# Kernel optimization log

Hardware: AMD Instinct MI355X
Metric: run time of the kernel (lower is better)

Reference implementation:

```python
import jax, jax.numpy as jnp
import numpy as np

B, S, D, H = 2, 4096, 512, 8
HD = D // H  # head_dim = 64


def setup_inputs() -> dict:
    key = jax.random.key(0)
    ks = jax.random.split(key, 7)
    scale = 1.0 / np.sqrt(D)
    return {
        "x": jax.random.normal(ks[0], (B, S, D), dtype=jnp.float32),
        "Wq": jax.random.uniform(ks[1], (D, D), jnp.float32, -scale, scale),
        "bq": jax.random.uniform(ks[2], (D,), jnp.float32, -scale, scale),
        "Wk": jax.random.uniform(ks[3], (D, D), jnp.float32, -scale, scale),
        "bk": jax.random.uniform(ks[4], (D,), jnp.float32, -scale, scale),
        "Wv": jax.random.uniform(ks[5], (D, D), jnp.float32, -scale, scale),
        "bv": jax.random.uniform(ks[6], (D,), jnp.float32, -scale, scale),
    }


def reference(x, Wq, bq, Wk, bk, Wv, bv):
    # torch Linear: y = x @ W.T + b
    q = x @ Wq.T + bq  # [B,S,D]
    k = x @ Wk.T + bk
    v = x @ Wv.T + bv
    # split heads -> [B,H,S,HD]
    q = q.reshape(B, S, H, HD).transpose(0, 2, 1, 3)
    k = k.reshape(B, S, H, HD).transpose(0, 2, 1, 3)
    v = v.reshape(B, S, H, HD).transpose(0, 2, 1, 3)
    # NOTE: module scales by sqrt(pitch_dim), NOT sqrt(head_dim) -- keep faithful.
    scores = jnp.einsum("bhqd,bhkd->bhqk", q, k) / jnp.sqrt(jnp.float32(D))
    causal = jnp.tril(jnp.ones((S, S), dtype=bool))  # lower-tri incl. diag allowed
    scores = jnp.where(causal, scores, -jnp.inf)
    attn = jax.nn.softmax(scores, axis=-1)
    out = jnp.einsum("bhqk,bhkd->bhqd", attn, v)  # [B,H,S,HD]
    return out.transpose(0, 2, 1, 3).reshape(B, S, D)
```

## Files before the change

### kernel.cpp

```cpp
#include <hip/hip_runtime.h>
#include <hip/hip_bf16.h>
#include <math.h>

#define BB 2
#define SS 4096
#define DD 512
#define HH 8
#define HD 64
#define MSD (BB*SS*DD)
#define WSZ (DD*DD)

#define XOFF (4*(size_t)MSD)
#define WOFF (5*(size_t)MSD)
#define POFF (3*(size_t)MSD)

typedef __attribute__((ext_vector_type(8))) short bf16x8;
typedef __attribute__((ext_vector_type(4))) float f32x4;

__device__ __forceinline__ unsigned short f2bf(float f) {
    unsigned int u = __float_as_uint(f);
    u += 0x7fff + ((u >> 16) & 1);
    return (unsigned short)(u >> 16);
}
__device__ __forceinline__ unsigned int pk2bf(float a, float b) {
    __hip_bfloat162 h = __float22bfloat162_rn(make_float2(a, b));
    union { __hip_bfloat162 h2; unsigned int u; } cv; cv.h2 = h;
    return cv.u;
}

#define GLD16(gsrc, ldst) \
    __builtin_amdgcn_global_load_lds((const __attribute__((address_space(1))) unsigned int*)(gsrc), \
                                     (__attribute__((address_space(3))) unsigned int*)(ldst), 16, 0, 0)

#define CH(qb,t0,t1) ((unsigned)(qb) | ((unsigned)(t0)<<8) | ((unsigned)(t1)<<16))
__device__ __constant__ unsigned int SCHED[48] = {
  CH(31,0,32),  CH(31,32,64), CH(0,0,2),
  CH(15,0,32),  CH(29,0,30),  CH(1,0,4),
  CH(29,30,60), CH(14,0,30),  CH(2,0,6),
  CH(28,0,29),  CH(28,29,58), CH(3,0,8),
  CH(27,0,28),  CH(13,0,28),  CH(4,0,10),
  CH(26,0,27),  CH(26,27,54), CH(5,0,12),
  CH(25,0,26),  CH(12,0,26),  CH(6,0,14),
  CH(24,0,25),  CH(24,25,50), CH(7,0,16),
  CH(30,0,31),  CH(17,0,18),  CH(16,0,17),
  CH(30,31,62), CH(17,18,36), CH(16,17,34),
  CH(27,28,56), CH(19,0,20),  CH(8,0,18),
  CH(25,26,52), CH(20,0,21),  CH(18,0,19),
  CH(23,0,24),  CH(22,0,23),  CH(18,19,38),
  CH(23,24,48), CH(21,0,22),  CH(19,20,40),
  CH(11,0,24),  CH(21,22,44), CH(9,0,20),
  CH(22,23,46), CH(10,0,22),  CH(20,21,42),
};

__global__ __launch_bounds__(256)
void convert_bf16(const float* __restrict__ x,
                  const float* __restrict__ Wq, const float* __restrict__ Wk,
                  const float* __restrict__ Wv, unsigned short* __restrict__ ws) {
    const int i8 = blockIdx.x*256 + threadIdx.x;
    const float* src; unsigned short* dst; size_t off;
    if (i8 < MSD/8) {
        src = x; dst = ws + XOFF; off = (size_t)i8 * 8;
    } else {
        size_t o = ((size_t)i8 - MSD/8) * 8;
        int wsel = (int)(o / WSZ);
        src = (wsel == 0) ? Wq : (wsel == 1) ? Wk : Wv;
        dst = ws + WOFF + (size_t)wsel*WSZ;
        off = o % WSZ;
    }
    float4 a = *(const float4*)&src[off];
    float4 b = *(const float4*)&src[off+4];
    unsigned short r[8] = { f2bf(a.x), f2bf(a.y), f2bf(a.z), f2bf(a.w),
                            f2bf(b.x), f2bf(b.y), f2bf(b.z), f2bf(b.w) };
    *(bf16x8*)&dst[off] = *(const bf16x8*)r;
}

__global__ __launch_bounds__(256)
void qkv_mfma(const float* __restrict__ bq, const float* __restrict__ bk,
              const float* __restrict__ bv, unsigned short* __restrict__ ws) {
    const int z = blockIdx.z;
    const unsigned short* Xb = ws + XOFF;
    const unsigned short* Wb = ws + WOFF + (size_t)z*WSZ;
    const float* bias = (z == 0) ? bq : (z == 1) ? bk : bv;
    unsigned short* dst = ws + (size_t)z*MSD;

    __shared__ __align__(16) unsigned short Sh[4*128*64];

    const int tid  = threadIdx.x;
    const int w    = tid >> 6, l = tid & 63;
    const int quad = l >> 4,  r16 = l & 15;
    const int wy   = w >> 1,  wx  = w & 1;
    const int m0   = blockIdx.y * 128;
    const int n0   = blockIdx.x * 128;

    const int srow   = l >> 3;
    const int schunk = (l & 7) ^ srow;

    f32x4 acc[4][4];
    #pragma unroll
    for (int i = 0; i < 4; ++i)
        #pragma unroll
        for (int j = 0; j < 4; ++j) acc[i][j] = (f32x4){0.f,0.f,0.f,0.f};

    #pragma unroll
    for (int u = 0; u < 4; ++u) {
        const int r0 = w*32 + u*8;
        GLD16(&Xb[(size_t)(m0 + r0 + srow)*DD + schunk*8], &Sh[r0*64]);
        GLD16(&Wb[(size_t)(n0 + r0 + srow)*DD + schunk*8], &Sh[16384 + r0*64]);
    }

    for (int kt = 0; kt < 8; ++kt) {
        __syncthreads();

        if (kt + 1 < 8) {
            const int k1 = (kt + 1)*64;
            const int b1 = (kt + 1) & 1;
            #pragma unroll
            for (int u = 0; u < 4; ++u) {
                const int r0 = w*32 + u*8;
                GLD16(&Xb[(size_t)(m0 + r0 + srow)*DD + k1 + schunk*8], &Sh[b1*8192 + r0*64]);
                GLD16(&Wb[(size_t)(n0 + r0 + srow)*DD + k1 + schunk*8], &Sh[16384 + b1*8192 + r0*64]);
            }
        }

        const unsigned short* Asb = Sh + (kt & 1)*8192;
        const unsigned short* Bsb = Sh + 16384 + (kt & 1)*8192;
        #pragma unroll
        for (int kc = 0; kc < 2; ++kc) {
            bf16x8 a[4], b[4];
            #pragma unroll
            for (int i = 0; i < 4; ++i) {
                const int mr = wy*64 + i*16 + r16;
                a[i] = *(const bf16x8*)&Asb[mr*64 + (((kc*4+quad) ^ (mr&7))*8)];
                const int nr = wx*64 + i*16 + r16;
                b[i] = *(const bf16x8*)&Bsb[nr*64 + (((kc*4+quad) ^ (nr&7))*8)];
            }
            __builtin_amdgcn_s_setprio(1);
            #pragma unroll
            for (int i = 0; i < 4; ++i)
                #pragma unroll
                for (int j = 0; j < 4; ++j) {
                    if (z == 2)
                        acc[i][j] = __builtin_amdgcn_mfma_f32_16x16x32_bf16(a[i], b[j], acc[i][j], 0, 0, 0);
                    else
                        acc[i][j] = __builtin_amdgcn_mfma_f32_16x16x32_bf16(b[j], a[i], acc[i][j], 0, 0, 0);
                }
            __builtin_amdgcn_s_setprio(0);
        }
    }

    __syncthreads();

    const float qscale = 0.04419417382415922f * 1.4426950408889634f;
    if (z == 2) {
        #pragma unroll
        for (int j = 0; j < 4; ++j) {
            const int nloc = wx*64 + j*16 + r16;
            const float bz = bias[n0 + nloc];
            #pragma unroll
            for (int i = 0; i < 4; ++i) {
                const int chunk = wy*8 + i*2 + (quad>>1);
                const int off   = (quad & 1) * 4;
                unsigned short r4[4];
                #pragma unroll
                for (int reg = 0; reg < 4; ++reg)
                    r4[reg] = f2bf(acc[i][j][reg] + bz);
                *(uint2*)&Sh[nloc*128 + ((chunk ^ (nloc & 7))*8) + off] = *(const uint2*)r4;
            }
        }
    } else {
        #pragma unroll
        for (int j = 0; j < 4; ++j) {
            const int nbase = wx*64 + j*16 + quad*4;
            const float4 bz4 = *(const float4*)&bias[n0 + nbase];
            const int chunk = wx*8 + j*2 + (quad>>1);
            const int off   = (quad & 1) * 4;
            #pragma unroll
            for (int i = 0; i < 4; ++i) {
                const int mloc = wy*64 + i*16 + r16;
                float v0 = acc[i][j][0] + bz4.x;
                float v1 = acc[i][j][1] + bz4.y;
                float v2 = acc[i][j][2] + bz4.z;
                float v3 = acc[i][j][3] + bz4.w;
                if (z == 0) { v0 *= qscale; v1 *= qscale; v2 *= qscale; v3 *= qscale; }
                unsigned short r4[4] = { f2bf(v0), f2bf(v1), f2bf(v2), f2bf(v3) };
                *(uint2*)&Sh[mloc*128 + ((chunk ^ (mloc & 7))*8) + off] = *(const uint2*)r4;
            }
        }
    }
    __syncthreads();

    if (z == 2) {
        const int b_ = m0 >> 12, s0_ = m0 & (SS-1);
        #pragma unroll
        for (int p = 0; p < 8; ++p) {
            const int f = p*256 + tid;
            const int nrow = f >> 4;
            const int mch  = f & 15;
            bf16x8 v = *(const bf16x8*)&Sh[nrow*128 + ((mch ^ (nrow & 7))*8)];
            const int ng = n0 + nrow;
            const int h = ng >> 6, hd = ng & 63;
            *(bf16x8*)&dst[((size_t)(b_*HH + h)*HD + hd)*SS + s0_ + mch*8] = v;
        }
    } else {
        #pragma unroll
        for (int p = 0; p < 8; ++p) {
            const int f = p*256 + tid;
            const int hh  = f >> 10;
            const int rem = f & 1023;
            const int sr  = rem >> 3;
            const int ch  = rem & 7;
            bf16x8 v = *(const bf16x8*)&Sh[sr*128 + (((hh*8 + ch) ^ (sr & 7))*8)];
            const int mg = m0 + sr;
            const int b_ = mg >> 12, s_ = mg & (SS-1);
            const int hg = (n0 >> 6) + hh;
            *(bf16x8*)&dst[((size_t)(b_*HH + hg)*SS + s_)*HD + ch*8] = v;
        }
    }
}

__global__ __launch_bounds__(512, 6)
void attn_mfma(unsigned short* __restrict__ ws, float* __restrict__ out) {
    const int bx = blockIdx.x;
    const int k_ = bx >> 8;
    const int j_ = bx & 255;
    const int bh = j_ & 15;
    const int ti = j_ >> 4;
    const unsigned int e = SCHED[ti*3 + k_];
    const int qb = e & 255;
    const int t0 = (e >> 8) & 255;
    const int t1 = (e >> 16) & 255;
    const int split = !(t0 == 0 && t1 == 2*qb + 2);
    const int half  = (t0 != 0);

    const int tid  = threadIdx.x;
    const int w    = tid >> 6, l = tid & 63;
    const int quad = l >> 4,  r16 = l & 15;
    const int qlo  = qb*128 + w*16;
    const int tdiag = 2*qb + (w >> 2);
    const int qoff  = (w & 3)*16;

    const unsigned short* Qg  = ws;
    const unsigned short* Kg  = ws + (size_t)MSD;
    const unsigned short* Vtg = ws + 2*(size_t)MSD;

    __shared__ __align__(16) unsigned short Ks[2][64*64];
    __shared__ __align__(16) unsigned short Vs[2][64*64];

    const size_t kbase = (size_t)bh*SS*HD;
    const size_t vbase = (size_t)bh*HD*SS;

    bf16x8 bqf[2];
    #pragma unroll
    for (int kc = 0; kc < 2; ++kc)
        bqf[kc] = *(const bf16x8*)&Qg[kbase + (size_t)(qlo + r16)*HD + kc*32 + quad*8];

    const f32x4 ZZ = (f32x4){0.f,0.f,0.f,0.f};
    const unsigned short onep[8] = {0x3F80,0x3F80,0x3F80,0x3F80,0x3F80,0x3F80,0x3F80,0x3F80};
    const bf16x8 ones8 = *(const bf16x8*)onep;

    f32x4 od[4];
    #pragma unroll
    for (int mt = 0; mt < 4; ++mt) od[mt] = ZZ;
    f32x4 lacc = ZZ;

    const int sr8 = l >> 3, sc = l & 7;
    const int srow = w*8 + sr8;
    const int scol = sc ^ (srow & 7);

    {
        const int jb0 = t0*64;
        GLD16(&Kg [kbase + (size_t)(jb0 + srow)*HD + scol*8], &Ks[0][(w*8)*64]);
        GLD16(&Vtg[vbase + (size_t)srow*SS + jb0 + scol*8],   &Vs[0][(w*8)*64]);
    }

    for (int t = t0; t < t1; ++t) {
        __syncthreads();

        if (t + 1 < t1) {
            const int jb1 = (t + 1)*64;
            const int b1  = (t + 1 - t0) & 1;
            GLD16(&Kg [kbase + (size_t)(jb1 + srow)*HD + scol*8], &Ks[b1][(w*8)*64]);
            GLD16(&Vtg[vbase + (size_t)srow*SS + jb1 + scol*8],   &Vs[b1][(w*8)*64]);
        }

        if (t <= tdiag) {
            const int bc = (t - t0) & 1;
            const unsigned short* Kb = Ks[bc];
            const unsigned short* Vb = Vs[bc];

            f32x4 z[4];
            __builtin_amdgcn_s_setprio(1);
            #pragma unroll
            for (int mt = 0; mt < 4; ++mt) {
                const int row = mt*16 + r16;
                bf16x8 ak0 = *(const bf16x8*)&Kb[row*64 + ((quad     ^ (row&7))*8)];
                bf16x8 ak1 = *(const bf16x8*)&Kb[row*64 + (((4+quad) ^ (row&7))*8)];
                z[mt] = __builtin_amdgcn_mfma_f32_16x16x32_bf16(ak0, bqf[0], ZZ, 0, 0, 0);
                z[mt] = __builtin_amdgcn_mfma_f32_16x16x32_bf16(ak1, bqf[1], z[mt], 0, 0, 0);
            }
            __builtin_amdgcn_s_setprio(0);

            if (t == tdiag) {
                #pragma unroll
                for (int mt = 0; mt < 4; ++mt)
                    #pragma unroll
                    for (int reg = 0; reg < 4; ++reg)
                        if (mt*16 + quad*4 + reg > qoff + r16)
                            z[mt][reg] = -1e30f;
            }

            unsigned int X0[4], X1[4];
            #pragma unroll
            for (int mt = 0; mt < 4; ++mt) {
                X0[mt] = pk2bf(__builtin_amdgcn_exp2f(z[mt][0]),
                               __builtin_amdgcn_exp2f(z[mt][1]));
                X1[mt] = pk2bf(__builtin_amdgcn_exp2f(z[mt][2]),
                               __builtin_amdgcn_exp2f(z[mt][3]));
            }

            bf16x8 pf[2];
            #pragma unroll
            for (int kc = 0; kc < 2; ++kc) {
                unsigned int a0 = X0[2*kc], b0 = X0[2*kc+1];
                unsigned int a1 = X1[2*kc], b1 = X1[2*kc+1];
                asm("v_permlane32_swap_b32 %0, %1" : "+v"(a0), "+v"(b0));
                asm("v_permlane16_swap_b32 %0, %1" : "+v"(a0), "+v"(b0));
                asm("v_permlane32_swap_b32 %0, %1" : "+v"(a1), "+v"(b1));
                asm("v_permlane16_swap_b32 %0, %1" : "+v"(a1), "+v"(b1));
                unsigned int wv[4] = { a0, a1, b0, b1 };
                pf[kc] = *(const bf16x8*)wv;
            }

            __builtin_amdgcn_s_setprio(1);
            lacc = __builtin_amdgcn_mfma_f32_16x16x32_bf16(ones8, pf[0], lacc, 0, 0, 0);
            lacc = __builtin_amdgcn_mfma_f32_16x16x32_bf16(ones8, pf[1], lacc, 0, 0, 0);
            #pragma unroll
            for (int mt = 0; mt < 4; ++mt) {
                const int row = mt*16 + r16;
                bf16x8 av0 = *(const bf16x8*)&Vb[row*64 + ((quad     ^ (row&7))*8)];
                bf16x8 av1 = *(const bf16x8*)&Vb[row*64 + (((4+quad) ^ (row&7))*8)];
                od[mt] = __builtin_amdgcn_mfma_f32_16x16x32_bf16(av0, pf[0], od[mt], 0, 0, 0);
                od[mt] = __builtin_amdgcn_mfma_f32_16x16x32_bf16(av1, pf[1], od[mt], 0, 0, 0);
            }
            __builtin_amdgcn_s_setprio(0);
        }
    }

    if (split) {
        const int p = 2*(bh*16 + (qb - 16)) + half;
        float* Op = (float*)(ws + POFF) + (size_t)p*(128*64);
        float* Lp = (float*)(ws + WOFF) + p*128;
        const int qloc = w*16 + r16;
        if (quad == 0) Lp[qloc] = lacc[0];
        #pragma unroll
        for (int mt = 0; mt < 4; ++mt)
            *(f32x4*)&Op[(size_t)qloc*64 + mt*16 + quad*4] = od[mt];
    } else {
        const int b_ = bh >> 3, h = bh & 7;
        const float inv = 1.0f / lacc[0];
        const int q = qlo + r16;
        float* op = out + ((size_t)(b_*SS + q))*DD + h*HD;
        #pragma unroll
        for (int mt = 0; mt < 4; ++mt) {
            float4 tt;
            tt.x = od[mt][0]*inv; tt.y = od[mt][1]*inv;
            tt.z = od[mt][2]*inv; tt.w = od[mt][3]*inv;
            *(float4*)&op[mt*16 + quad*4] = tt;
        }
    }
}

__global__ __launch_bounds__(256)
void attn_combine(const unsigned short* __restrict__ ws, float* __restrict__ out) {
    const int i  = blockIdx.x*256 + threadIdx.x;
    const int d4 = i & 15;
    const int q  = (i >> 4) & 127;
    const int r  = i >> 11;
    const int bh = r >> 4, qb = 16 + (r & 15);

    const float* Opart = (const float*)(ws + POFF);
    const float* Lpart = (const float*)(ws + WOFF);

    const float4 a = *(const float4*)&Opart[((size_t)(2*r)*128 + q)*64 + d4*4];
    const float4 b = *(const float4*)&Opart[((size_t)(2*r + 1)*128 + q)*64 + d4*4];
    const float lt = Lpart[(2*r)*128 + q] + Lpart[(2*r + 1)*128 + q];
    const float inv = 1.0f / lt;

    const int qg = qb*128 + q;
    const int b_ = bh >> 3, h = bh & 7;
    float4 o;
    o.x = (a.x + b.x)*inv; o.y = (a.y + b.y)*inv;
    o.z = (a.z + b.z)*inv; o.w = (a.w + b.w)*inv;
    *(float4*)&out[((size_t)(b_*SS + qg))*DD + h*HD + d4*4] = o;
}

extern "C" void kernel_launch(void* const* d_in, const int* in_sizes, int n_in,
                              void* d_out, int out_size, void* d_ws, size_t ws_size,
                              hipStream_t stream) {
    const float* x  = (const float*)d_in[0];
    const float* Wq = (const float*)d_in[1];
    const float* bq = (const float*)d_in[2];
    const float* Wk = (const float*)d_in[3];
    const float* bk = (const float*)d_in[4];
    const float* Wv = (const float*)d_in[5];
    const float* bv = (const float*)d_in[6];
    float* out = (float*)d_out;
    unsigned short* ws = (unsigned short*)d_ws;

    const int nconv = (MSD/8 + 3*WSZ/8 + 255) / 256;
    convert_bf16<<<nconv, 256, 0, stream>>>(x, Wq, Wk, Wv, ws);

    dim3 ggrid(DD/128, (BB*SS)/128, 3);
    qkv_mfma<<<ggrid, 256, 0, stream>>>(bq, bk, bv, ws);

    attn_mfma<<<768, 512, 0, stream>>>(ws, out);
    attn_combine<<<2048, 256, 0, stream>>>(ws, out);
}
```

Before: 156.2 us.

## Fuse Q, K, V projections into one kernel sharing the X tile

Replaces the three-way grid-z QKV GEMM with a single 512-thread kernel in which each block loads its X tile once and multiplies it against all three weight tiles, keeping three accumulator sets. This cuts X global and LDS traffic by a factor of three and reduces the block count. In exchange the kernel uses more registers and LDS per block (four double-buffered tiles), runs 256 blocks instead of 768, and serialises the three epilogues through one shared staging buffer with extra barriers.

```diff
diff --git a/kernel.cpp b/kernel.cpp
--- a/kernel.cpp
+++ b/kernel.cpp
@@ -74,147 +74,161 @@
     *(bf16x8*)&dst[off] = *(const bf16x8*)r;
 }
 
-__global__ __launch_bounds__(256)
-void qkv_mfma(const float* __restrict__ bq, const float* __restrict__ bk,
-              const float* __restrict__ bv, unsigned short* __restrict__ ws) {
-    const int z = blockIdx.z;
+__global__ __launch_bounds__(512, 2)
+void qkv_fused(const float* __restrict__ bq, const float* __restrict__ bk,
+               const float* __restrict__ bv, unsigned short* __restrict__ ws) {
     const unsigned short* Xb = ws + XOFF;
-    const unsigned short* Wb = ws + WOFF + (size_t)z*WSZ;
-    const float* bias = (z == 0) ? bq : (z == 1) ? bk : bv;
-    unsigned short* dst = ws + (size_t)z*MSD;
-
-    __shared__ __align__(16) unsigned short Sh[4*128*64];
+    const unsigned short* Wz0 = ws + WOFF;
+    const unsigned short* Wz1 = ws + WOFF + WSZ;
+    const unsigned short* Wz2 = ws + WOFF + 2*(size_t)WSZ;
+
+    __shared__ __align__(16) unsigned short As[2][128*64];
+    __shared__ __align__(16) unsigned short Bs[3][2][128*64];
 
     const int tid  = threadIdx.x;
     const int w    = tid >> 6, l = tid & 63;
     const int quad = l >> 4,  r16 = l & 15;
-    const int wy   = w >> 1,  wx  = w & 1;
+    const int wm   = w >> 2,  wn  = w & 3;
+    const int n0   = blockIdx.x * 128;
     const int m0   = blockIdx.y * 128;
-    const int n0   = blockIdx.x * 128;
-
-    const int srow   = l >> 3;
-    const int schunk = (l & 7) ^ srow;
-
-    f32x4 acc[4][4];
+
+    const int sr8 = l >> 3, sc = l & 7;
+
+    f32x4 acc[3][4][2];
     #pragma unroll
-    for (int i = 0; i < 4; ++i)
+    for (int z = 0; z < 3; ++z)
         #pragma unroll
-        for (int j = 0; j < 4; ++j) acc[i][j] = (f32x4){0.f,0.f,0.f,0.f};
+        for (int i = 0; i < 4; ++i)
+            #pragma unroll
+            for (int j = 0; j < 2; ++j) acc[z][i][j] = (f32x4){0.f,0.f,0.f,0.f};
+
+    auto STAGE = [&](int k0, int b) {
+        #pragma unroll
+        for (int u = 0; u < 2; ++u) {
+            const int r0  = w*16 + u*8;
+            const int row = r0 + sr8;
+            const int c   = sc ^ (row & 7);
+            GLD16(&Xb [(size_t)(m0 + row)*DD + k0 + c*8], &As[b][r0*64]);
+            GLD16(&Wz0[(size_t)(n0 + row)*DD + k0 + c*8], &Bs[0][b][r0*64]);
+            GLD16(&Wz1[(size_t)(n0 + row)*DD + k0 + c*8], &Bs[1][b][r0*64]);
+            GLD16(&Wz2[(size_t)(n0 + row)*DD + k0 + c*8], &Bs[2][b][r0*64]);
+        }
+    };
+
+    STAGE(0, 0);
 
     #pragma unroll
-    for (int u = 0; u < 4; ++u) {
-        const int r0 = w*32 + u*8;
-        GLD16(&Xb[(size_t)(m0 + r0 + srow)*DD + schunk*8], &Sh[r0*64]);
-        GLD16(&Wb[(size_t)(n0 + r0 + srow)*DD + schunk*8], &Sh[16384 + r0*64]);
-    }
-
     for (int kt = 0; kt < 8; ++kt) {
         __syncthreads();
-
-        if (kt + 1 < 8) {
-            const int k1 = (kt + 1)*64;
-            const int b1 = (kt + 1) & 1;
-            #pragma unroll
-            for (int u = 0; u < 4; ++u) {
-                const int r0 = w*32 + u*8;
-                GLD16(&Xb[(size_t)(m0 + r0 + srow)*DD + k1 + schunk*8], &Sh[b1*8192 + r0*64]);
-                GLD16(&Wb[(size_t)(n0 + r0 + srow)*DD + k1 + schunk*8], &Sh[16384 + b1*8192 + r0*64]);
-            }
-        }
-
-        const unsigned short* Asb = Sh + (kt & 1)*8192;
-        const unsigned short* Bsb = Sh + 16384 + (kt & 1)*8192;
+        if (kt + 1 < 8) STAGE((kt + 1)*64, (kt + 1) & 1);
+
+        const int bb = kt & 1;
         #pragma unroll
         for (int kc = 0; kc < 2; ++kc) {
-            bf16x8 a[4], b[4];
+            bf16x8 a[4];
             #pragma unroll
             for (int i = 0; i < 4; ++i) {
-                const int mr = wy*64 + i*16 + r16;
-                a[i] = *(const bf16x8*)&Asb[mr*64 + (((kc*4+quad) ^ (mr&7))*8)];
-                const int nr = wx*64 + i*16 + r16;
-                b[i] = *(const bf16x8*)&Bsb[nr*64 + (((kc*4+quad) ^ (nr&7))*8)];
+                const int mr = wm*64 + i*16 + r16;
+                a[i] = *(const bf16x8*)&As[bb][mr*64 + (((kc*4+quad) ^ (mr&7))*8)];
+            }
+            bf16x8 b0[2], b1[2], b2[2];
+            #pragma unroll
+            for (int j = 0; j < 2; ++j) {
+                const int nr = wn*32 + j*16 + r16;
+                const int sw = ((kc*4+quad) ^ (nr&7))*8;
+                b0[j] = *(const bf16x8*)&Bs[0][bb][nr*64 + sw];
+                b1[j] = *(const bf16x8*)&Bs[1][bb][nr*64 + sw];
+                b2[j] = *(const bf16x8*)&Bs[2][bb][nr*64 + sw];
             }
             __builtin_amdgcn_s_setprio(1);
             #pragma unroll
             for (int i = 0; i < 4; ++i)
                 #pragma unroll
-                for (int j = 0; j < 4; ++j) {
-                    if (z == 2)
-                        acc[i][j] = __builtin_amdgcn_mfma_f32_16x16x32_bf16(a[i], b[j], acc[i][j], 0, 0, 0);
-                    else
-                        acc[i][j] = __builtin_amdgcn_mfma_f32_16x16x32_bf16(b[j], a[i], acc[i][j], 0, 0, 0);
+                for (int j = 0; j < 2; ++j) {
+                    acc[0][i][j] = __builtin_amdgcn_mfma_f32_16x16x32_bf16(b0[j], a[i], acc[0][i][j], 0, 0, 0);
+                    acc[1][i][j] = __builtin_amdgcn_mfma_f32_16x16x32_bf16(b1[j], a[i], acc[1][i][j], 0, 0, 0);
+                    acc[2][i][j] = __builtin_amdgcn_mfma_f32_16x16x32_bf16(a[i], b2[j], acc[2][i][j], 0, 0, 0);
                 }
             __builtin_amdgcn_s_setprio(0);
         }
     }
 
     __syncthreads();
-
+    unsigned short* Ct = &As[0][0];
     const float qscale = 0.04419417382415922f * 1.4426950408889634f;
-    if (z == 2) {
-        #pragma unroll
-        for (int j = 0; j < 4; ++j) {
-            const int nloc = wx*64 + j*16 + r16;
-            const float bz = bias[n0 + nloc];
-            #pragma unroll
-            for (int i = 0; i < 4; ++i) {
-                const int chunk = wy*8 + i*2 + (quad>>1);
+    const float* biases[3] = { bq, bk, bv };
+
+    #pragma unroll
+    for (int z = 0; z < 3; ++z) {
+        unsigned short* dst = ws + (size_t)z*MSD;
+        const float* bias = biases[z];
+
+        if (z == 2) {
+            #pragma unroll
+            for (int j = 0; j < 2; ++j) {
+                const int nloc = wn*32 + j*16 + r16;
+                const float bz = bias[n0 + nloc];
+                #pragma unroll
+                for (int i = 0; i < 4; ++i) {
+                    const int chunk = wm*8 + i*2 + (quad>>1);
+                    const int off   = (quad & 1) * 4;
+                    unsigned short r4[4];
+                    #pragma unroll
+                    for (int reg = 0; reg < 4; ++reg)
+                        r4[reg] = f2bf(acc[2][i][j][reg] + bz);
+                    *(uint2*)&Ct[nloc*128 + ((chunk ^ (nloc & 7))*8) + off] = *(const uint2*)r4;
+                }
+            }
+        } else {
+            #pragma unroll
+            for (int j = 0; j < 2; ++j) {
+                const int nbase = wn*32 + j*16 + quad*4;
+                const float4 bz4 = *(const float4*)&bias[n0 + nbase];
+                const int chunk = wn*4 + j*2 + (quad>>1);
                 const int off   = (quad & 1) * 4;
-                unsigned short r4[4];
                 #pragma unroll
-                for (int reg = 0; reg < 4; ++reg)
-                    r4[reg] = f2bf(acc[i][j][reg] + bz);
-                *(uint2*)&Sh[nloc*128 + ((chunk ^ (nloc & 7))*8) + off] = *(const uint2*)r4;
-            }
-        }
-    } else {
-        #pragma unroll
-        for (int j = 0; j < 4; ++j) {
-            const int nbase = wx*64 + j*16 + quad*4;
-            const float4 bz4 = *(const float4*)&bias[n0 + nbase];
-            const int chunk = wx*8 + j*2 + (quad>>1);
-            const int off   = (quad & 1) * 4;
-            #pragma unroll
-            for (int i = 0; i < 4; ++i) {
-                const int mloc = wy*64 + i*16 + r16;
-                float v0 = acc[i][j][0] + bz4.x;
-                float v1 = acc[i][j][1] + bz4.y;
-                float v2 = acc[i][j][2] + bz4.z;
-                float v3 = acc[i][j][3] + bz4.w;
-                if (z == 0) { v0 *= qscale; v1 *= qscale; v2 *= qscale; v3 *= qscale; }
-                unsigned short r4[4] = { f2bf(v0), f2bf(v1), f2bf(v2), f2bf(v3) };
-                *(uint2*)&Sh[mloc*128 + ((chunk ^ (mloc & 7))*8) + off] = *(const uint2*)r4;
-            }
-        }
-    }
-    __syncthreads();
-
-    if (z == 2) {
-        const int b_ = m0 >> 12, s0_ = m0 & (SS-1);
-        #pragma unroll
-        for (int p = 0; p < 8; ++p) {
-            const int f = p*256 + tid;
-            const int nrow = f >> 4;
-            const int mch  = f & 15;
-            bf16x8 v = *(const bf16x8*)&Sh[nrow*128 + ((mch ^ (nrow & 7))*8)];
-            const int ng = n0 + nrow;
-            const int h = ng >> 6, hd = ng & 63;
-            *(bf16x8*)&dst[((size_t)(b_*HH + h)*HD + hd)*SS + s0_ + mch*8] = v;
-        }
-    } else {
-        #pragma unroll
-        for (int p = 0; p < 8; ++p) {
-            const int f = p*256 + tid;
-            const int hh  = f >> 10;
-            const int rem = f & 1023;
-            const int sr  = rem >> 3;
-            const int ch  = rem & 7;
-            bf16x8 v = *(const bf16x8*)&Sh[sr*128 + (((hh*8 + ch) ^ (sr & 7))*8)];
-            const int mg = m0 + sr;
-            const int b_ = mg >> 12, s_ = mg & (SS-1);
-            const int hg = (n0 >> 6) + hh;
-            *(bf16x8*)&dst[((size_t)(b_*HH + hg)*SS + s_)*HD + ch*8] = v;
-        }
+                for (int i = 0; i < 4; ++i) {
+                    const int mloc = wm*64 + i*16 + r16;
+                    float v0 = acc[z][i][j][0] + bz4.x;
+                    float v1 = acc[z][i][j][1] + bz4.y;
+                    float v2 = acc[z][i][j][2] + bz4.z;
+                    float v3 = acc[z][i][j][3] + bz4.w;
+                    if (z == 0) { v0 *= qscale; v1 *= qscale; v2 *= qscale; v3 *= qscale; }
+                    unsigned short r4[4] = { f2bf(v0), f2bf(v1), f2bf(v2), f2bf(v3) };
+                    *(uint2*)&Ct[mloc*128 + ((chunk ^ (mloc & 7))*8) + off] = *(const uint2*)r4;
+                }
+            }
+        }
+        __syncthreads();
+
+        if (z == 2) {
+            const int b_ = m0 >> 12, s0_ = m0 & (SS-1);
+            #pragma unroll
+            for (int p = 0; p < 4; ++p) {
+                const int f = p*512 + tid;
+                const int nrow = f >> 4;
+                const int mch  = f & 15;
+                bf16x8 v = *(const bf16x8*)&Ct[nrow*128 + ((mch ^ (nrow & 7))*8)];
+                const int ng = n0 + nrow;
+                const int h = ng >> 6, hd = ng & 63;
+                *(bf16x8*)&dst[((size_t)(b_*HH + h)*HD + hd)*SS + s0_ + mch*8] = v;
+            }
+        } else {
+            #pragma unroll
+            for (int p = 0; p < 4; ++p) {
+                const int f = p*512 + tid;
+                const int hh  = f >> 10;
+                const int rem = f & 1023;
+                const int sr  = rem >> 3;
+                const int ch  = rem & 7;
+                bf16x8 v = *(const bf16x8*)&Ct[sr*128 + (((hh*8 + ch) ^ (sr & 7))*8)];
+                const int mg = m0 + sr;
+                const int b_ = mg >> 12, s_ = mg & (SS-1);
+                const int hg = (n0 >> 6) + hh;
+                *(bf16x8*)&dst[((size_t)(b_*HH + hg)*SS + s_)*HD + ch*8] = v;
+            }
+        }
+        if (z < 2) __syncthreads();
     }
 }
 
@@ -410,8 +424,8 @@
     const int nconv = (MSD/8 + 3*WSZ/8 + 255) / 256;
     convert_bf16<<<nconv, 256, 0, stream>>>(x, Wq, Wk, Wv, ws);
 
-    dim3 ggrid(DD/128, (BB*SS)/128, 3);
-    qkv_mfma<<<ggrid, 256, 0, stream>>>(bq, bk, bv, ws);
+    dim3 ggrid(DD/128, (BB*SS)/128);
+    qkv_fused<<<ggrid, 512, 0, stream>>>(bq, bk, bv, ws);
 
     attn_mfma<<<768, 512, 0, stream>>>(ws, out);
     attn_combine<<<2048, 256, 0, stream>>>(ws, out);
```

Result: faster. 152.2 us (-2.6%).
